# Performance work log

Hardware: AMD Instinct MI355X
Metric: run time of the kernel (lower is better)

## Reference

```python
import jax, jax.numpy as jnp
import numpy as np
import math

N_HEAD = 16
ROPE_BASE = 10000.0


def _rope_as_in_source(x):
    """Faithful replication of RotaryPositionalEmbeddings.forward applied to
    x of shape [B, H, T, hd] (called after transpose in the source, so
    seq_len = x.size(1) = H: angles are indexed by head index, not position)."""
    B, H, T, hd = x.shape
    theta = 1.0 / (ROPE_BASE ** (jnp.arange(0, hd, 2, dtype=jnp.float32) / hd))  # [hd/2]
    ang = jnp.arange(H, dtype=jnp.float32)[:, None] * theta[None, :]  # [H, hd/2]
    cos = jnp.cos(ang)[None, :, None, :]  # [1, H, 1, hd/2]
    sin = jnp.sin(ang)[None, :, None, :]
    xr = x.reshape(B, H, T, hd // 2, 2)
    out = jnp.stack([
        xr[..., 0] * cos - xr[..., 1] * sin,
        xr[..., 1] * cos + xr[..., 0] * sin,
    ], axis=-1)
    return out.reshape(B, H, T, hd)


def setup_inputs() -> dict:
    key = jax.random.key(0)
    ks = jax.random.split(key, 5)
    B, T, C = 2, 2048, 1024
    s = 0.02
    return {
        "x": jax.random.normal(ks[0], (B, T, C), dtype=jnp.float32),
        "W_attn": jax.random.normal(ks[1], (C, 3 * C), dtype=jnp.float32) * s,
        "b_attn": jnp.zeros((3 * C,), dtype=jnp.float32),
        "W_proj": jax.random.normal(ks[2], (C, C), dtype=jnp.float32) * s,
        "b_proj": jnp.zeros((C,), dtype=jnp.float32),
    }


def reference(x, W_attn, b_attn, W_proj, b_proj):
    B, T, C = x.shape
    H = N_HEAD
    hd = C // H
    qkv = x @ W_attn + b_attn  # [B, T, 3C]
    q, k, v = jnp.split(qkv, 3, axis=2)
    # [B, T, H, hd] -> [B, H, T, hd]
    q = q.reshape(B, T, H, hd).transpose(0, 2, 1, 3)
    k = k.reshape(B, T, H, hd).transpose(0, 2, 1, 3)
    v = v.reshape(B, T, H, hd).transpose(0, 2, 1, 3)
    q = _rope_as_in_source(q)
    k = _rope_as_in_source(k)
    att = jnp.einsum("bhqd,bhkd->bhqk", q, k) * (1.0 / math.sqrt(hd))
    causal = jnp.tril(jnp.ones((T, T), dtype=bool))
    att = jnp.where(causal[None, None, :, :], att, -jnp.inf)
    att = jax.nn.softmax(att, axis=-1)
    y = jnp.einsum("bhqk,bhkd->bhqd", att, v)  # [B, H, T, hd]
    y = y.transpose(0, 2, 1, 3).reshape(B, T, C)
    return y @ W_proj + b_proj
```

## Files before the change

kernel.cpp:

```cpp
#include <hip/hip_runtime.h>

typedef __attribute__((ext_vector_type(8))) short bf16x8;
typedef __attribute__((ext_vector_type(4))) float f32x4;
typedef __attribute__((ext_vector_type(4))) unsigned int uint4v;
typedef unsigned short ushort_t;

#define BB 2
#define TT 2048
#define CC 1024
#define HH 16
#define HD 64
#define MM (BB * TT)
#define N3C (3 * CC)
#define KD 1024
#define NT64 16

__device__ __forceinline__ ushort_t f2b(float f) {
  unsigned u = __builtin_bit_cast(unsigned, f);
  u += 0x7fffu + ((u >> 16) & 1u);
  return (ushort_t)(u >> 16);
}

__device__ __forceinline__ unsigned pack2rne(float a, float b) {
  return (unsigned)f2b(a) | ((unsigned)f2b(b) << 16);
}

__device__ __forceinline__ unsigned pack2bf(float a, float b) {
  unsigned ua = (__builtin_bit_cast(unsigned, a) + 0x8000u) >> 16;
  unsigned ub = (__builtin_bit_cast(unsigned, b) + 0x8000u) & 0xffff0000u;
  return ua | ub;
}

__device__ __forceinline__ float fexp2(float x) {
#if __has_builtin(__builtin_amdgcn_exp2f)
  return __builtin_amdgcn_exp2f(x);
#else
  return __expf(x * 0.6931471805599453f);
#endif
}

__device__ __forceinline__ f32x4 mfma16(bf16x8 a, bf16x8 b, f32x4 c) {
  return __builtin_amdgcn_mfma_f32_16x16x32_bf16(a, b, c, 0, 0, 0);
}

__device__ __forceinline__ void load_lds16(const void* g, void* l) {
  __builtin_amdgcn_global_load_lds((const __attribute__((address_space(1))) void*)g,
                                   (__attribute__((address_space(3))) void*)l, 16, 0, 0);
}

#define BAR()   __builtin_amdgcn_s_barrier()
#define SB0()   __builtin_amdgcn_sched_barrier(0)
#define LGKM0() asm volatile("s_waitcnt lgkmcnt(0)" ::: "memory")

using lds_p = const __attribute__((address_space(3))) ushort_t*;
template <int OFF>
__device__ __forceinline__ bf16x8 dsr128o(lds_p a) {
  bf16x8 r;
  asm volatile("ds_read_b128 %0, %1 offset:%2" : "=v"(r) : "v"(a), "i"(OFF));
  return r;
}
#define RD4(dst, base, off0)                                                   \
  dst[0] = dsr128o<(off0)>(base);        dst[1] = dsr128o<(off0) + 1024>(base);\
  dst[2] = dsr128o<(off0) + 2048>(base); dst[3] = dsr128o<(off0) + 3072>(base);

__global__ __launch_bounds__(256) void prep(const float* __restrict__ x,
                                            const float* __restrict__ Wa,
                                            const float* __restrict__ Wp,
                                            ushort_t* __restrict__ xb,
                                            ushort_t* __restrict__ wat,
                                            ushort_t* __restrict__ wpt) {
  const int blk = blockIdx.x, tid = threadIdx.x;
  if (blk < 4096) {
    int i = blk * 256 + tid;
    const float4 v = ((const float4*)x)[i];
    typedef __attribute__((ext_vector_type(4))) ushort_t us4;
    us4 r;
    r.x = f2b(v.x); r.y = f2b(v.y); r.z = f2b(v.z); r.w = f2b(v.w);
    ((us4*)xb)[i] = r;
    return;
  }
  __shared__ ushort_t tile[32][33];
  const float* W; ushort_t* Wt; int R, Nc, n0, r0;
  if (blk < 7168) {
    int tb = blk - 4096;
    W = Wa; Wt = wat; R = CC; Nc = N3C;
    n0 = (tb % 96) * 32; r0 = (tb / 96) * 32;
  } else {
    int tb = blk - 7168;
    W = Wp; Wt = wpt; R = CC; Nc = CC;
    n0 = (tb & 31) * 32; r0 = (tb >> 5) * 32;
  }
  const int c = tid & 31, rr = tid >> 5;
#pragma unroll
  for (int i = 0; i < 4; ++i) {
    int r = rr + i * 8;
    tile[r][c] = f2b(W[(size_t)(r0 + r) * Nc + n0 + c]);
  }
  __syncthreads();
#pragma unroll
  for (int i = 0; i < 4; ++i) {
    int r = rr + i * 8;
    Wt[(size_t)(n0 + r) * R + r0 + c] = tile[c][r];
  }
}

__global__ __launch_bounds__(512, 2) void qkv256(const ushort_t* __restrict__ A,
                                                 const ushort_t* __restrict__ Bt,
                                                 const float* __restrict__ bias,
                                                 ushort_t* __restrict__ qo,
                                                 ushort_t* __restrict__ ko,
                                                 ushort_t* __restrict__ vto) {
  extern __shared__ ushort_t lds[];
  ushort_t* As = lds;
  ushort_t* Bs = lds + 32768;

  const int tid = threadIdx.x, lane = tid & 63, wave = tid >> 6;
  const int l15 = lane & 15, quad = lane >> 4;
  const int wm = (wave >> 2) * 128, wn = (wave & 3) * 64;

  const int bid = blockIdx.y * 12 + blockIdx.x;
  const int xcd = bid & 7, idx = bid >> 3;
  const int by = (xcd >> 1) * 4 + idx / 6;
  const int bx = (xcd & 1) * 6 + idx % 6;
  const int m0 = by * 256, n0 = bx * 256;

  const int rw0 = tid >> 2, gc0 = (tid & 3) ^ ((rw0 >> 1) & 3);
  const ushort_t* sA0 = A + (size_t)(m0 + rw0) * KD + gc0 * 8;
  const ushort_t* sA1 = sA0 + (size_t)128 * KD;
  const ushort_t* sB0 = Bt + (size_t)(n0 + rw0) * KD + gc0 * 8;
  const ushort_t* sB1 = sB0 + (size_t)128 * KD;
  ushort_t* dA0 = As + tid * 8;
  ushort_t* dA1 = dA0 + 4096;
  ushort_t* dB0 = Bs + tid * 8;
  ushort_t* dB1 = dB0 + 4096;

  auto stA = [&](int tau, int kh) {
    const int so = ((tau & 1) * 2 + kh) * 8192;
    const int ko2 = tau * 64 + kh * 32;
    load_lds16(sA0 + ko2, dA0 + so);
    load_lds16(sA1 + ko2, dA1 + so);
  };
  auto stB = [&](int tau, int kh) {
    const int so = ((tau & 1) * 2 + kh) * 8192;
    const int ko2 = tau * 64 + kh * 32;
    load_lds16(sB0 + ko2, dB0 + so);
    load_lds16(sB1 + ko2, dB1 + so);
  };

  const int swc = (quad ^ ((l15 >> 1) & 3)) * 8;
  const int rdA = (wm + l15) * 32 + swc;
  const int rdB = (wn + l15) * 32 + swc;
  lds_p A3 = (lds_p)As;
  lds_p B3 = (lds_p)Bs;

  f32x4 acc[8][4] = {};

  stB(0, 0); stA(0, 0); stB(0, 1); stA(0, 1);
  stB(1, 0); stA(1, 0); stB(1, 1);
  asm volatile("s_waitcnt vmcnt(6)" ::: "memory");
  BAR();
  SB0();

  bf16x8 a[4], b0[4], b1[4];
  for (int t = 0; t < NT64; ++t) {
    const int par = t & 1;
    lds_p pA = A3 + par * 16384 + rdA;
    lds_p pB = B3 + par * 16384 + rdB;

    RD4(b0, pB, 0);
    RD4(a, pA, 0);
    if (t + 1 < NT64) stA(t + 1, 1);
    BAR();
    LGKM0();
    SB0();
    __builtin_amdgcn_s_setprio(1);
#pragma unroll
    for (int i = 0; i < 4; ++i)
#pragma unroll
      for (int j = 0; j < 4; ++j) acc[i][j] = mfma16(a[i], b0[j], acc[i][j]);
    __builtin_amdgcn_s_setprio(0);
    BAR();
    SB0();

    RD4(a, pA, 4096);
    if (t + 2 < NT64) stB(t + 2, 0);
    BAR();
    LGKM0();
    SB0();
    __builtin_amdgcn_s_setprio(1);
#pragma unroll
    for (int i = 0; i < 4; ++i)
#pragma unroll
      for (int j = 0; j < 4; ++j) acc[4 + i][j] = mfma16(a[i], b0[j], acc[4 + i][j]);
    __builtin_amdgcn_s_setprio(0);
    BAR();
    SB0();

    RD4(b1, pB, 16384);
    RD4(a, pA, 16384);
    if (t + 2 < NT64) stA(t + 2, 0);
    BAR();
    LGKM0();
    SB0();
    __builtin_amdgcn_s_setprio(1);
#pragma unroll
    for (int i = 0; i < 4; ++i)
#pragma unroll
      for (int j = 0; j < 4; ++j) acc[i][j] = mfma16(a[i], b1[j], acc[i][j]);
    __builtin_amdgcn_s_setprio(0);
    BAR();
    SB0();

    RD4(a, pA, 16384 + 4096);
    if (t + 2 < NT64) stB(t + 2, 1);
    if (t < NT64 - 2)       { asm volatile("s_waitcnt vmcnt(6)" ::: "memory"); }
    else if (t == NT64 - 2) { asm volatile("s_waitcnt vmcnt(0)" ::: "memory"); }
    BAR();
    LGKM0();
    SB0();
    __builtin_amdgcn_s_setprio(1);
#pragma unroll
    for (int i = 0; i < 4; ++i)
#pragma unroll
      for (int j = 0; j < 4; ++j) acc[4 + i][j] = mfma16(a[i], b1[j], acc[4 + i][j]);
    __builtin_amdgcn_s_setprio(0);
    BAR();
    SB0();
  }

  float bv[4];
#pragma unroll
  for (int j = 0; j < 4; ++j) bv[j] = bias[n0 + wn + j * 16 + l15];

  const int h8 = l15 >> 3, j8l = l15 & 7;
  const int t0 = (m0 + wm) & 2047, b = (m0 + wm) >> 11;
  const int gsec = (n0 + wn) >> 10, h = ((n0 + wn) & 1023) >> 6;
  const int bh = b * HH + h;
  if (gsec < 2) {
    ushort_t* dst = (gsec == 0 ? qo + ((size_t)bh * 128 + (t0 >> 4)) * 1024
                               : ko + ((size_t)bh * 32 + (t0 >> 6)) * 4096)
                    + h8 * 128 + quad * 32 + j8l;
#pragma unroll
    for (int i = 0; i < 8; ++i)
#pragma unroll
      for (int j = 0; j < 4; ++j)
#pragma unroll
        for (int r = 0; r < 4; ++r)
          dst[i * 1024 + (j >> 1) * 512 + (j & 1) * 256 + r * 8] =
              f2b(acc[i][j][r] + bv[j]);
  } else {
    ushort_t* dst = vto + ((size_t)bh * 32 + (t0 >> 6)) * 4096 + quad * 128 + l15 * 8;
#pragma unroll
    for (int j = 0; j < 4; ++j)
#pragma unroll
      for (int i = 0; i < 8; ++i) {
        uint2 u;
        u.x = pack2rne(acc[i][j][0] + bv[j], acc[i][j][1] + bv[j]);
        u.y = pack2rne(acc[i][j][2] + bv[j], acc[i][j][3] + bv[j]);
        const int il = i & 3;
        *(uint2*)&dst[(i >> 2) * 4096 + j * 1024 + (il >> 1) * 512 + (il & 1) * 4] = u;
      }
  }
}

template <int EPI, int NT>
__global__ __launch_bounds__(256) void gemm_bt(const ushort_t* __restrict__ A,
                                               const ushort_t* __restrict__ Bt,
                                               const float* __restrict__ bias,
                                               ushort_t* __restrict__ qo,
                                               ushort_t* __restrict__ ko,
                                               ushort_t* __restrict__ vto,
                                               float* __restrict__ outp,
                                               int N, int K) {
  constexpr int NJ = NT / 32;
  __shared__ __align__(16) ushort_t As[128 * 64];
  __shared__ __align__(16) ushort_t Bs[NT * 64];
  const int tid = threadIdx.x, lane = tid & 63, wave = tid >> 6;
  const int l15 = lane & 15, quad = lane >> 4;
  const int wm = (wave >> 1) * 64, wn = (wave & 1) * (NT / 2);
  const int m0 = blockIdx.y * 128, n0 = blockIdx.x * NT;

  f32x4 acc[4][NJ] = {};
  for (int k0 = 0; k0 < K; k0 += 64) {
    __syncthreads();
#pragma unroll
    for (int p = 0; p < 4; ++p) {
      int d16 = p * 256 + tid;
      int pan = d16 >> 9, rem = d16 & 511, row = rem >> 2, cc = rem & 3;
      load_lds16(&A[(size_t)(m0 + row) * K + k0 + pan * 32 + cc * 8], &As[d16 * 8]);
    }
#pragma unroll
    for (int p = 0; p < NT / 32; ++p) {
      int d16 = p * 256 + tid;
      int pan = d16 / (NT * 4), rem = d16 % (NT * 4), row = rem >> 2, cc = rem & 3;
      load_lds16(&Bt[(size_t)(n0 + row) * K + k0 + pan * 32 + cc * 8], &Bs[d16 * 8]);
    }
    __syncthreads();
#pragma unroll
    for (int pan = 0; pan < 2; ++pan) {
      const ushort_t* Ap = &As[pan * 4096];
      const ushort_t* Bp = &Bs[pan * (NT * 32)];
      bf16x8 af[4], bfr[NJ];
#pragma unroll
      for (int i = 0; i < 4; ++i)
        af[i] = *(const bf16x8*)&Ap[(wm + i * 16 + l15) * 32 + quad * 8];
#pragma unroll
      for (int j = 0; j < NJ; ++j)
        bfr[j] = *(const bf16x8*)&Bp[(wn + j * 16 + l15) * 32 + quad * 8];
#pragma unroll
      for (int i = 0; i < 4; ++i)
#pragma unroll
        for (int j = 0; j < NJ; ++j)
          acc[i][j] = mfma16(af[i], bfr[j], acc[i][j]);
    }
  }

  float bv[NJ];
#pragma unroll
  for (int j = 0; j < NJ; ++j) bv[j] = bias[n0 + wn + j * 16 + l15];

  if (EPI == 1) {
#pragma unroll
    for (int i = 0; i < 4; ++i)
#pragma unroll
      for (int r = 0; r < 4; ++r) {
        float* rp = outp + (size_t)(m0 + wm + i * 16 + quad * 4 + r) * N + n0 + wn + l15;
#pragma unroll
        for (int j = 0; j < NJ; ++j) rp[j * 16] = acc[i][j][r] + bv[j];
      }
  }
}

__global__ __launch_bounds__(256) void attn_kernel(const ushort_t* __restrict__ Qf,
                                                   const ushort_t* __restrict__ Kf,
                                                   const ushort_t* __restrict__ Vf,
                                                   ushort_t* __restrict__ y) {
  __shared__ __align__(16) float red[2][2176];
  const int tid = threadIdx.x, lane = tid & 63, wave = tid >> 6;
  const int l15 = lane & 15, quad = lane >> 4;
  const int idx = blockIdx.x;
  const int xcd = idx & 7, j = idx >> 3;
  const int bh = xcd * 4 + (j & 3);
  const int g = 63 - (j >> 2);
  const int qs = g * 32;
  const int nk = (qs + 95) >> 6;

  const float SCL = 0.125f * 1.4426950408889634f;

  const ushort_t* qbase = Qf + (((size_t)bh * 128 + (qs >> 4)) * 2 * 64 + lane) * 8;
  bf16x8 qf[2][2];
#pragma unroll
  for (int st = 0; st < 2; ++st)
#pragma unroll
    for (int dh = 0; dh < 2; ++dh)
      qf[st][dh] = *(const bf16x8*)(qbase + (st * 2 + dh) * 512);

  f32x4 o[2][4] = {};
  float l_r[2] = {0.f, 0.f};

  for (int it = wave; it < nk; it += 4) {
    const bool diag = (it == nk - 1);
    const size_t tb = ((size_t)bh * 32 + it) * 4096 + (size_t)lane * 8;
    bf16x8 kf[4][2], vf[4][2];
#pragma unroll
    for (int ng = 0; ng < 4; ++ng)
#pragma unroll
      for (int dh = 0; dh < 2; ++dh)
        kf[ng][dh] = *(const bf16x8*)(Kf + tb + (ng * 2 + dh) * 512);
#pragma unroll
    for (int dg = 0; dg < 4; ++dg)
#pragma unroll
      for (int h = 0; h < 2; ++h)
        vf[dg][h] = *(const bf16x8*)(Vf + tb + (dg * 2 + h) * 512);

#pragma unroll
    for (int st = 0; st < 2; ++st) {
      f32x4 s[4];
#pragma unroll
      for (int ng = 0; ng < 4; ++ng) {
        f32x4 z = {};
        z = mfma16(kf[ng][0], qf[st][0], z);
        z = mfma16(kf[ng][1], qf[st][1], z);
        s[ng] = z;
      }
      float p[4][4];
      const int qg = qs + st * 16 + l15;
#pragma unroll
      for (int ng = 0; ng < 4; ++ng)
#pragma unroll
        for (int r = 0; r < 4; ++r) {
          float pv = fexp2(s[ng][r] * SCL);
          if (diag) {
            int kg = it * 64 + ng * 16 + quad * 4 + r;
            pv = (kg > qg) ? 0.f : pv;
          }
          p[ng][r] = pv;
          l_r[st] += pv;
        }
      union { uint4v u; bf16x8 v; } pk0, pk1;
      pk0.u[0] = pack2bf(p[0][0], p[0][1]); pk0.u[1] = pack2bf(p[0][2], p[0][3]);
      pk0.u[2] = pack2bf(p[1][0], p[1][1]); pk0.u[3] = pack2bf(p[1][2], p[1][3]);
      pk1.u[0] = pack2bf(p[2][0], p[2][1]); pk1.u[1] = pack2bf(p[2][2], p[2][3]);
      pk1.u[2] = pack2bf(p[3][0], p[3][1]); pk1.u[3] = pack2bf(p[3][2], p[3][3]);
#pragma unroll
      for (int dg = 0; dg < 4; ++dg) {
        o[st][dg] = mfma16(vf[dg][0], pk0.v, o[st][dg]);
        o[st][dg] = mfma16(vf[dg][1], pk1.v, o[st][dg]);
      }
    }
  }

  auto dump = [&](float* buf) {
#pragma unroll
    for (int st = 0; st < 2; ++st)
#pragma unroll
      for (int dg = 0; dg < 4; ++dg)
        *(f32x4*)&buf[(st * 4 + dg) * 256 + lane * 4] = o[st][dg];
    buf[2048 + lane * 2 + 0] = l_r[0];
    buf[2048 + lane * 2 + 1] = l_r[1];
  };
  auto merge = [&](const float* buf) {
#pragma unroll
    for (int st = 0; st < 2; ++st)
#pragma unroll
      for (int dg = 0; dg < 4; ++dg)
        o[st][dg] += *(const f32x4*)&buf[(st * 4 + dg) * 256 + lane * 4];
    l_r[0] += buf[2048 + lane * 2 + 0];
    l_r[1] += buf[2048 + lane * 2 + 1];
  };
  if (wave == 1) dump(red[0]);
  if (wave == 3) dump(red[1]);
  __syncthreads();
  if (wave == 0) merge(red[0]);
  if (wave == 2) merge(red[1]);
  __syncthreads();
  if (wave == 2) dump(red[0]);
  __syncthreads();
  if (wave == 0) {
    merge(red[0]);
    const int b = bh >> 4, h = bh & 15;
#pragma unroll
    for (int st = 0; st < 2; ++st) {
      float lf = l_r[st];
      lf += __shfl_xor(lf, 16);
      lf += __shfl_xor(lf, 32);
      const float inv = 1.0f / lf;
      const size_t row = (size_t)(b * TT + qs + st * 16 + l15) * CC;
#pragma unroll
      for (int dg = 0; dg < 4; ++dg) {
        uint2 u;
        u.x = pack2rne(o[st][dg][0] * inv, o[st][dg][1] * inv);
        u.y = pack2rne(o[st][dg][2] * inv, o[st][dg][3] * inv);
        *(uint2*)&y[row + h * HD + dg * 16 + quad * 4] = u;
      }
    }
  }
}

extern "C" void kernel_launch(void* const* d_in, const int* in_sizes, int n_in,
                              void* d_out, int out_size, void* d_ws, size_t ws_size,
                              hipStream_t stream) {
  const float* x  = (const float*)d_in[0];
  const float* Wa = (const float*)d_in[1];
  const float* ba = (const float*)d_in[2];
  const float* Wp = (const float*)d_in[3];
  const float* bp = (const float*)d_in[4];
  float* out = (float*)d_out;

  char* ws = (char*)d_ws;
  ushort_t* xb  = (ushort_t*)(ws + 0);
  ushort_t* wat = (ushort_t*)(ws + 8388608);
  ushort_t* wpt = (ushort_t*)(ws + 14680064);
  ushort_t* Qf  = (ushort_t*)(ws + 16777216);
  ushort_t* Kf  = (ushort_t*)(ws + 25165824);
  ushort_t* Vf  = (ushort_t*)(ws + 33554432);
  ushort_t* yb  = (ushort_t*)(ws + 41943040);

  static int attr_done = 0;
  if (!attr_done) {
    (void)hipFuncSetAttribute((const void*)qkv256,
                              hipFuncAttributeMaxDynamicSharedMemorySize, 131072);
    attr_done = 1;
  }

  prep<<<8192, 256, 0, stream>>>(x, Wa, Wp, xb, wat, wpt);

  qkv256<<<dim3(N3C / 256, MM / 256), 512, 131072, stream>>>(xb, wat, ba, Qf, Kf, Vf);

  attn_kernel<<<2048, 256, 0, stream>>>(Qf, Kf, Vf, yb);

  gemm_bt<1, 64><<<dim3(CC / 64, MM / 128), 256, 0, stream>>>(
      yb, wpt, bp, nullptr, nullptr, nullptr, out, CC, CC);
}
```

Baseline: 172.8 us.

## Restructure QKV GEMM mainloop into 4-stage ring with one barrier per k-step

Replaces the QKV projection GEMM's two-slot, four-phase-per-iteration schedule, which had many barriers and full lgkmcnt(0) waits, with a 4-slot ring of 32-wide k-tiles. Each iteration issues one barrier and prefetches three tiles ahead. All A/B fragments for the step are issued up front, and each MFMA group waits with a graded lgkmcnt so the math overlaps the remaining LDS reads. This is meant to cut barrier and synchronisation stalls in the mainloop. In exchange it uses more registers for the fragments and depends on correct vmcnt accounting across the deeper prefetch.

After: 173.4 us. Within noise of the previous version (+0.3%).

```diff
diff --git a/kernel.cpp b/kernel.cpp
--- a/kernel.cpp
+++ b/kernel.cpp
@@ -13,7 +13,7 @@
 #define MM (BB * TT)
 #define N3C (3 * CC)
 #define KD 1024
-#define NT64 16
+#define NT32 32
 
 __device__ __forceinline__ ushort_t f2b(float f) {
   unsigned u = __builtin_bit_cast(unsigned, f);
@@ -50,7 +50,6 @@
 
 #define BAR()   __builtin_amdgcn_s_barrier()
 #define SB0()   __builtin_amdgcn_sched_barrier(0)
-#define LGKM0() asm volatile("s_waitcnt lgkmcnt(0)" ::: "memory")
 
 using lds_p = const __attribute__((address_space(3))) ushort_t*;
 template <int OFF>
@@ -59,9 +58,6 @@
   asm volatile("ds_read_b128 %0, %1 offset:%2" : "=v"(r) : "v"(a), "i"(OFF));
   return r;
 }
-#define RD4(dst, base, off0)                                                   \
-  dst[0] = dsr128o<(off0)>(base);        dst[1] = dsr128o<(off0) + 1024>(base);\
-  dst[2] = dsr128o<(off0) + 2048>(base); dst[3] = dsr128o<(off0) + 3072>(base);
 
 __global__ __launch_bounds__(256) void prep(const float* __restrict__ x,
                                             const float* __restrict__ Wa,
@@ -134,15 +130,11 @@
   ushort_t* dB0 = Bs + tid * 8;
   ushort_t* dB1 = dB0 + 4096;
 
-  auto stA = [&](int tau, int kh) {
-    const int so = ((tau & 1) * 2 + kh) * 8192;
-    const int ko2 = tau * 64 + kh * 32;
+  auto stage = [&](int tt) {
+    const int so = (tt & 3) * 8192;
+    const int ko2 = tt * 32;
     load_lds16(sA0 + ko2, dA0 + so);
     load_lds16(sA1 + ko2, dA1 + so);
-  };
-  auto stB = [&](int tau, int kh) {
-    const int so = ((tau & 1) * 2 + kh) * 8192;
-    const int ko2 = tau * 64 + kh * 32;
     load_lds16(sB0 + ko2, dB0 + so);
     load_lds16(sB1 + ko2, dB1 + so);
   };
@@ -155,78 +147,53 @@
 
   f32x4 acc[8][4] = {};
 
-  stB(0, 0); stA(0, 0); stB(0, 1); stA(0, 1);
-  stB(1, 0); stA(1, 0); stB(1, 1);
-  asm volatile("s_waitcnt vmcnt(6)" ::: "memory");
-  BAR();
-  SB0();
-
-  bf16x8 a[4], b0[4], b1[4];
-  for (int t = 0; t < NT64; ++t) {
-    const int par = t & 1;
-    lds_p pA = A3 + par * 16384 + rdA;
-    lds_p pB = B3 + par * 16384 + rdB;
-
-    RD4(b0, pB, 0);
-    RD4(a, pA, 0);
-    if (t + 1 < NT64) stA(t + 1, 1);
-    BAR();
-    LGKM0();
-    SB0();
-    __builtin_amdgcn_s_setprio(1);
-#pragma unroll
-    for (int i = 0; i < 4; ++i)
-#pragma unroll
-      for (int j = 0; j < 4; ++j) acc[i][j] = mfma16(a[i], b0[j], acc[i][j]);
-    __builtin_amdgcn_s_setprio(0);
+  stage(0); stage(1); stage(2);
+
+#define GRP(i, N)                                                  \
+  asm volatile("s_waitcnt lgkmcnt(" #N ")" ::: "memory");          \
+  SB0();                                                           \
+  acc[i][0] = mfma16(a[i], b[0], acc[i][0]);                       \
+  acc[i][1] = mfma16(a[i], b[1], acc[i][1]);                       \
+  acc[i][2] = mfma16(a[i], b[2], acc[i][2]);                       \
+  acc[i][3] = mfma16(a[i], b[3], acc[i][3]);
+
+  for (int t = 0; t < NT32; ++t) {
+    if (t <= NT32 - 3)       { asm volatile("s_waitcnt vmcnt(8)" ::: "memory"); }
+    else if (t == NT32 - 2)  { asm volatile("s_waitcnt vmcnt(4)" ::: "memory"); }
+    else                     { asm volatile("s_waitcnt vmcnt(0)" ::: "memory"); }
     BAR();
     SB0();
-
-    RD4(a, pA, 4096);
-    if (t + 2 < NT64) stB(t + 2, 0);
-    BAR();
-    LGKM0();
+    if (t + 3 < NT32) stage(t + 3);
+
+    lds_p pA = A3 + (t & 3) * 8192 + rdA;
+    lds_p pB = B3 + (t & 3) * 8192 + rdB;
+    bf16x8 a[8], b[4];
+    a[0] = dsr128o<0>(pA);
+    b[0] = dsr128o<0>(pB);
+    b[1] = dsr128o<1024>(pB);
+    b[2] = dsr128o<2048>(pB);
+    b[3] = dsr128o<3072>(pB);
+    a[1] = dsr128o<1024>(pA);
+    a[2] = dsr128o<2048>(pA);
+    a[3] = dsr128o<3072>(pA);
+    a[4] = dsr128o<4096>(pA);
+    a[5] = dsr128o<5120>(pA);
+    a[6] = dsr128o<6144>(pA);
+    a[7] = dsr128o<7168>(pA);
+
+    __builtin_amdgcn_s_setprio(1);
+    GRP(0, 7)
+    GRP(1, 6)
+    GRP(2, 5)
+    GRP(3, 4)
+    GRP(4, 3)
+    GRP(5, 2)
+    GRP(6, 1)
+    GRP(7, 0)
+    __builtin_amdgcn_s_setprio(0);
     SB0();
-    __builtin_amdgcn_s_setprio(1);
-#pragma unroll
-    for (int i = 0; i < 4; ++i)
-#pragma unroll
-      for (int j = 0; j < 4; ++j) acc[4 + i][j] = mfma16(a[i], b0[j], acc[4 + i][j]);
-    __builtin_amdgcn_s_setprio(0);
-    BAR();
-    SB0();
-
-    RD4(b1, pB, 16384);
-    RD4(a, pA, 16384);
-    if (t + 2 < NT64) stA(t + 2, 0);
-    BAR();
-    LGKM0();
-    SB0();
-    __builtin_amdgcn_s_setprio(1);
-#pragma unroll
-    for (int i = 0; i < 4; ++i)
-#pragma unroll
-      for (int j = 0; j < 4; ++j) acc[i][j] = mfma16(a[i], b1[j], acc[i][j]);
-    __builtin_amdgcn_s_setprio(0);
-    BAR();
-    SB0();
-
-    RD4(a, pA, 16384 + 4096);
-    if (t + 2 < NT64) stB(t + 2, 1);
-    if (t < NT64 - 2)       { asm volatile("s_waitcnt vmcnt(6)" ::: "memory"); }
-    else if (t == NT64 - 2) { asm volatile("s_waitcnt vmcnt(0)" ::: "memory"); }
-    BAR();
-    LGKM0();
-    SB0();
-    __builtin_amdgcn_s_setprio(1);
-#pragma unroll
-    for (int i = 0; i < 4; ++i)
-#pragma unroll
-      for (int j = 0; j < 4; ++j) acc[4 + i][j] = mfma16(a[i], b1[j], acc[4 + i][j]);
-    __builtin_amdgcn_s_setprio(0);
-    BAR();
-    SB0();
-  }
+  }
+#undef GRP
 
   float bv[4];
 #pragma unroll
```
